# Optimization experiments

Measured on AMD Instinct MI355X. Metric: run time of the kernel, lower is better.

## Reference

```python
import jax, jax.numpy as jnp
import numpy as np

S = 8            # num_residual_streams (power of 2)
K = 3            # number of 2x2 Kronecker factors = log2(S)
T = 2 * K        # total_res_coeffs (2 permutations per 2x2 factor)
D = 2048         # feature dim per stream
B = 2            # batch
N = 1024         # sequence length


def setup_inputs() -> dict:
    key = jax.random.key(0)
    ks = jax.random.split(key, 6)
    residuals = jax.random.normal(ks[0], (B * S, N, D), dtype=jnp.float32)
    gamma = jnp.zeros((S * D,), dtype=jnp.float32)  # RMSNorm gamma (init zeros as in source)
    static_alpha = jax.random.normal(ks[1], (S + T,), dtype=jnp.float32)
    W_alpha = jax.random.normal(ks[2], (S * D, S + T), dtype=jnp.float32) * 0.02
    pre_branch_scale = jnp.full((1,), 0.01, dtype=jnp.float32)
    residual_scale = jnp.full((1,), 0.01, dtype=jnp.float32)
    static_beta = jax.random.normal(ks[3], (S,), dtype=jnp.float32)
    W_beta = jax.random.normal(ks[4], (S * D, S), dtype=jnp.float32) * 0.02
    h_post_scale = jnp.asarray(0.01, dtype=jnp.float32)
    return {"residuals": residuals, "gamma": gamma, "static_alpha": static_alpha,
            "W_alpha": W_alpha, "pre_branch_scale": pre_branch_scale,
            "residual_scale": residual_scale, "static_beta": static_beta,
            "W_beta": W_beta, "h_post_scale": h_post_scale}


def _kron_2x2(p):
    # p: (..., K) prob of identity for each 2x2 factor; U_k = [[p,1-p],[1-p,p]]
    q = 1.0 - p
    mats = jnp.stack([jnp.stack([p, q], axis=-1),
                      jnp.stack([q, p], axis=-1)], axis=-2)  # (..., K, 2, 2)
    out = mats[..., 0, :, :]
    for k in range(1, K):  # loop over fixed small K (structural), not data dims
        m = mats[..., k, :, :]
        a1, a2 = out.shape[-2], out.shape[-1]
        out = (out[..., :, None, :, None] * m[..., None, :, None, :]).reshape(
            *out.shape[:-2], a1 * 2, a2 * 2)
    return out  # (..., S, S) doubly stochastic Kronecker Hres


def reference(residuals, gamma, static_alpha, W_alpha, pre_branch_scale,
              residual_scale, static_beta, W_beta, h_post_scale):
    # residuals: (B*S, N, D) with stream-major layout '(b s) n d'
    r = residuals.reshape(B, S, N, D).transpose(0, 2, 1, 3)       # (B, N, S, D)
    flat = r.reshape(B, N, S * D)
    # RMSNorm: F.normalize(x, dim=-1) * sqrt(dim) * (gamma + 1)
    inv = jax.lax.rsqrt(jnp.maximum(jnp.sum(flat * flat, axis=-1, keepdims=True), 1e-24))
    normed = flat * inv * np.float32(np.sqrt(S * D)) * (gamma + 1.0)
    # dynamic-alpha projection: first S cols -> H_pre, last T cols -> Hres coeffs
    coeffs = normed @ W_alpha                                     # (B, N, S + T)
    dyn_pre, dyn_res = coeffs[..., :S], coeffs[..., S:]
    static_pre, static_res = static_alpha[:S], static_alpha[S:]
    # H_pre: softmax over streams -> convex-combination branch input
    w_pre = jax.nn.softmax(pre_branch_scale * dyn_pre + static_pre, axis=-1)
    branch_input = jnp.einsum('bns,bnsd->bnd', w_pre, r)
    # H_res: Kronecker product of 2x2 doubly-stochastic factor matrices
    cr = (residual_scale * dyn_res + static_res).reshape(B, N, K, 2)
    p = jax.nn.softmax(cr, axis=-1)[..., 0]                       # (B, N, K)
    hres = _kron_2x2(p)                                           # (B, N, S, S)
    mixed = jnp.einsum('bnst,bnsd->bntd', hres, r)                # stream mixing
    # branch = identity; depth connection with sigmoid-gated beta (H_post)
    beta = jax.nn.sigmoid(h_post_scale * (normed @ W_beta) + static_beta)  # (B, N, S)
    out = mixed + beta[..., None] * branch_input[..., None, :]    # (B, N, S, D)
    return out.transpose(0, 2, 1, 3).reshape(B * S, N, D)
```

## Files before the change

### kernel.cpp

```cpp
#include <hip/hip_runtime.h>
#include <stdint.h>

#define S_  8
#define D_  2048
#define B_  2
#define N_  1024
#define SD_ 16384
#define JP_ 11

__device__ __forceinline__ unsigned pack_bf16_rne(float a, float b) {
    unsigned ua = __float_as_uint(a);
    unsigned ub = __float_as_uint(b);
    ua += 0x7FFFu + ((ua >> 16) & 1u);
    ub += 0x7FFFu + ((ub >> 16) & 1u);
    return (ua >> 16) | (ub & 0xFFFF0000u);
}

extern "C" __global__ void krom_prep(const float* __restrict__ gamma,
                                     const float* __restrict__ Wa,
                                     const float* __restrict__ Wb,
                                     unsigned* __restrict__ Wp)
{
    const int u = blockIdx.x * 256 + threadIdx.x;
    if (u >= JP_ * SD_) return;
    const int sj = u >> 11;
    const int d  = u & 2047;
    const int s  = sj / JP_;
    const int jp = sj - s * JP_;
    const int i  = (s << 11) + d;
    const float g = gamma[i] + 1.0f;
    float w0, w1;
    if (jp < 7) {
        w0 = Wa[i * 14 + 2 * jp];
        w1 = Wa[i * 14 + 2 * jp + 1];
    } else {
        const int j = jp - 7;
        w0 = Wb[i * 8 + 2 * j];
        w1 = Wb[i * 8 + 2 * j + 1];
    }
    Wp[u] = pack_bf16_rne(g * w0, g * w1);
}

extern "C" __global__ void __launch_bounds__(512, 2)
krom_fused(const float* __restrict__ res,
           const unsigned* __restrict__ Wp,
           const float* __restrict__ sa,
           const float* __restrict__ pre_s,
           const float* __restrict__ res_s,
           const float* __restrict__ sb,
           const float* __restrict__ hps,
           float* __restrict__ out)
{
    const int tid = threadIdx.x;
    const int blk = blockIdx.x;
    const int b   = blk >> 9;
    const int n0  = (blk & 511) * 2;
    const int d0  = tid * 4;

    float acc0[23], acc1[23];
#pragma unroll
    for (int j = 0; j < 23; ++j) { acc0[j] = 0.0f; acc1[j] = 0.0f; }

    for (int s = 0; s < S_; ++s) {
        const float* pr = res + (((size_t)(b * S_ + s) * N_ + n0) * D_ + d0);
        const float4 va = *reinterpret_cast<const float4*>(pr);
        const float4 vb = *reinterpret_cast<const float4*>(pr + D_);
        const float ra[4] = {va.x, va.y, va.z, va.w};
        const float rb[4] = {vb.x, vb.y, vb.z, vb.w};
#pragma unroll
        for (int k = 0; k < 4; ++k) {
            acc0[22] = fmaf(ra[k], ra[k], acc0[22]);
            acc1[22] = fmaf(rb[k], rb[k], acc1[22]);
        }
        const unsigned* pw = Wp + ((s * JP_) << 11) + d0;
#pragma unroll
        for (int jp = 0; jp < JP_; ++jp) {
            const uint4 u = *reinterpret_cast<const uint4*>(pw + (jp << 11));
            const unsigned uu[4] = {u.x, u.y, u.z, u.w};
#pragma unroll
            for (int k = 0; k < 4; ++k) {
                const float w0 = __uint_as_float(uu[k] << 16);
                const float w1 = __uint_as_float(uu[k] & 0xFFFF0000u);
                acc0[2 * jp]     = fmaf(ra[k], w0, acc0[2 * jp]);
                acc0[2 * jp + 1] = fmaf(ra[k], w1, acc0[2 * jp + 1]);
                acc1[2 * jp]     = fmaf(rb[k], w0, acc1[2 * jp]);
                acc1[2 * jp + 1] = fmaf(rb[k], w1, acc1[2 * jp + 1]);
            }
        }
    }

    __shared__ float red[8][2][23];
    __shared__ float fin[2][23];
    const int wave = tid >> 6, lane = tid & 63;
#pragma unroll
    for (int j = 0; j < 23; ++j) {
        float v0 = acc0[j], v1 = acc1[j];
#pragma unroll
        for (int m = 1; m < 64; m <<= 1) {
            v0 += __shfl_xor(v0, m, 64);
            v1 += __shfl_xor(v1, m, 64);
        }
        if (lane == 0) { red[wave][0][j] = v0; red[wave][1][j] = v1; }
    }
    __syncthreads();
    if (tid < 46) {
        const int n = tid / 23, j = tid - n * 23;
        float v = 0.0f;
#pragma unroll
        for (int w = 0; w < 8; ++w) v += red[w][n][j];
        fin[n][j] = v;
    }
    __syncthreads();

    __shared__ float wpre[2][S_], bet[2][S_], pk3[2][3];
    if (tid < 2) {
        const int n = tid;
        const float inv   = rsqrtf(fmaxf(fin[n][22], 1e-24f));
        const float scale = inv * 128.0f;
        float c[22];
#pragma unroll
        for (int j = 0; j < 22; ++j) c[j] = fin[n][j] * scale;
        const float ps = pre_s[0], rs = res_s[0], hs = hps[0];
        float lg[8], mx = -1e30f;
#pragma unroll
        for (int s = 0; s < 8; ++s) { lg[s] = ps * c[s] + sa[s]; mx = fmaxf(mx, lg[s]); }
        float sum = 0.0f;
#pragma unroll
        for (int s = 0; s < 8; ++s) { lg[s] = expf(lg[s] - mx); sum += lg[s]; }
        const float rsum = 1.0f / sum;
#pragma unroll
        for (int s = 0; s < 8; ++s) wpre[n][s] = lg[s] * rsum;
#pragma unroll
        for (int k = 0; k < 3; ++k) {
            float a0 = rs * c[8 + 2 * k] + sa[8 + 2 * k];
            float a1 = rs * c[9 + 2 * k] + sa[9 + 2 * k];
            pk3[n][k] = 1.0f / (1.0f + expf(a1 - a0));
        }
#pragma unroll
        for (int t = 0; t < 8; ++t)
            bet[n][t] = 1.0f / (1.0f + expf(-(hs * c[14 + t] + sb[t])));
    }
    __syncthreads();

    __shared__ float Ms[2][S_][S_];
    if (tid < 128) {
        const int n = tid >> 6, e = tid & 63, s = e >> 3, t = e & 7;
        float h = 1.0f;
#pragma unroll
        for (int k = 0; k < 3; ++k) {
            int sbit = (s >> (2 - k)) & 1, tbit = (t >> (2 - k)) & 1;
            float pk = pk3[n][k];
            h *= (sbit == tbit) ? pk : (1.0f - pk);
        }
        Ms[n][s][t] = h + bet[n][t] * wpre[n][s];
    }
    __syncthreads();

#pragma unroll
    for (int n = 0; n < 2; ++n) {
        float o[8][4];
#pragma unroll
        for (int t = 0; t < 8; ++t)
#pragma unroll
            for (int k = 0; k < 4; ++k) o[t][k] = 0.0f;

        for (int s = 0; s < S_; ++s) {
            const float4 rv = *reinterpret_cast<const float4*>(
                res + (((size_t)(b * S_ + s) * N_ + (n0 + n)) * D_ + d0));
            const float4 m0 = *reinterpret_cast<const float4*>(&Ms[n][s][0]);
            const float4 m1 = *reinterpret_cast<const float4*>(&Ms[n][s][4]);
            o[0][0] = fmaf(m0.x, rv.x, o[0][0]); o[0][1] = fmaf(m0.x, rv.y, o[0][1]);
            o[0][2] = fmaf(m0.x, rv.z, o[0][2]); o[0][3] = fmaf(m0.x, rv.w, o[0][3]);
            o[1][0] = fmaf(m0.y, rv.x, o[1][0]); o[1][1] = fmaf(m0.y, rv.y, o[1][1]);
            o[1][2] = fmaf(m0.y, rv.z, o[1][2]); o[1][3] = fmaf(m0.y, rv.w, o[1][3]);
            o[2][0] = fmaf(m0.z, rv.x, o[2][0]); o[2][1] = fmaf(m0.z, rv.y, o[2][1]);
            o[2][2] = fmaf(m0.z, rv.z, o[2][2]); o[2][3] = fmaf(m0.z, rv.w, o[2][3]);
            o[3][0] = fmaf(m0.w, rv.x, o[3][0]); o[3][1] = fmaf(m0.w, rv.y, o[3][1]);
            o[3][2] = fmaf(m0.w, rv.z, o[3][2]); o[3][3] = fmaf(m0.w, rv.w, o[3][3]);
            o[4][0] = fmaf(m1.x, rv.x, o[4][0]); o[4][1] = fmaf(m1.x, rv.y, o[4][1]);
            o[4][2] = fmaf(m1.x, rv.z, o[4][2]); o[4][3] = fmaf(m1.x, rv.w, o[4][3]);
            o[5][0] = fmaf(m1.y, rv.x, o[5][0]); o[5][1] = fmaf(m1.y, rv.y, o[5][1]);
            o[5][2] = fmaf(m1.y, rv.z, o[5][2]); o[5][3] = fmaf(m1.y, rv.w, o[5][3]);
            o[6][0] = fmaf(m1.z, rv.x, o[6][0]); o[6][1] = fmaf(m1.z, rv.y, o[6][1]);
            o[6][2] = fmaf(m1.z, rv.z, o[6][2]); o[6][3] = fmaf(m1.z, rv.w, o[6][3]);
            o[7][0] = fmaf(m1.w, rv.x, o[7][0]); o[7][1] = fmaf(m1.w, rv.y, o[7][1]);
            o[7][2] = fmaf(m1.w, rv.z, o[7][2]); o[7][3] = fmaf(m1.w, rv.w, o[7][3]);
        }
#pragma unroll
        for (int t = 0; t < 8; ++t) {
            float* po = out + (((size_t)(b * S_ + t) * N_ + (n0 + n)) * D_ + d0);
            *reinterpret_cast<float4*>(po) = make_float4(o[t][0], o[t][1], o[t][2], o[t][3]);
        }
    }
}

extern "C" void kernel_launch(void* const* d_in, const int* in_sizes, int n_in,
                              void* d_out, int out_size, void* d_ws, size_t ws_size,
                              hipStream_t stream)
{
    (void)in_sizes; (void)n_in; (void)out_size; (void)ws_size;
    const float* residuals = (const float*)d_in[0];
    const float* gamma     = (const float*)d_in[1];
    const float* sa        = (const float*)d_in[2];
    const float* Wa        = (const float*)d_in[3];
    const float* pre_s     = (const float*)d_in[4];
    const float* res_s     = (const float*)d_in[5];
    const float* sb        = (const float*)d_in[6];
    const float* Wb        = (const float*)d_in[7];
    const float* hps       = (const float*)d_in[8];

    unsigned* Wp = (unsigned*)d_ws;

    hipLaunchKernelGGL(krom_prep, dim3((JP_ * SD_ + 255) / 256), dim3(256), 0, stream,
                       gamma, Wa, Wb, Wp);
    hipLaunchKernelGGL(krom_fused, dim3(B_ * N_ / 2), dim3(512), 0, stream,
                       residuals, Wp, sa, pre_s, res_s, sb, hps, (float*)d_out);
}
```

Before: 305.5 us.

## Process four tokens per block and use nontemporal output stores

Each block now handles four sequence positions instead of two, so every bf16 weight load feeds twice as many FMAs. This halves weight traffic per token and halves the grid to 512 blocks. Output writes switch to nontemporal stores so streaming output does not pollute the cache before residuals are re-read. The cost is more accumulator registers (92 versus 46), which may hurt occupancy under launch_bounds(512,2) and risks spilling, and fewer blocks to fill the GPU.

Result: no change. 304.4 us (-0.4%).

```diff
diff --git a/kernel.cpp b/kernel.cpp
--- a/kernel.cpp
+++ b/kernel.cpp
@@ -7,6 +7,9 @@
 #define N_  1024
 #define SD_ 16384
 #define JP_ 11
+#define NP_ 4
+
+typedef float f32x4 __attribute__((ext_vector_type(4)));
 
 __device__ __forceinline__ unsigned pack_bf16_rne(float a, float b) {
     unsigned ua = __float_as_uint(a);
@@ -53,24 +56,26 @@
 {
     const int tid = threadIdx.x;
     const int blk = blockIdx.x;
-    const int b   = blk >> 9;
-    const int n0  = (blk & 511) * 2;
+    const int b   = blk >> 8;
+    const int n0  = (blk & 255) * NP_;
     const int d0  = tid * 4;
 
-    float acc0[23], acc1[23];
-#pragma unroll
-    for (int j = 0; j < 23; ++j) { acc0[j] = 0.0f; acc1[j] = 0.0f; }
+    float acc[NP_][23];
+#pragma unroll
+    for (int n = 0; n < NP_; ++n)
+#pragma unroll
+        for (int j = 0; j < 23; ++j) acc[n][j] = 0.0f;
 
     for (int s = 0; s < S_; ++s) {
         const float* pr = res + (((size_t)(b * S_ + s) * N_ + n0) * D_ + d0);
-        const float4 va = *reinterpret_cast<const float4*>(pr);
-        const float4 vb = *reinterpret_cast<const float4*>(pr + D_);
-        const float ra[4] = {va.x, va.y, va.z, va.w};
-        const float rb[4] = {vb.x, vb.y, vb.z, vb.w};
-#pragma unroll
-        for (int k = 0; k < 4; ++k) {
-            acc0[22] = fmaf(ra[k], ra[k], acc0[22]);
-            acc1[22] = fmaf(rb[k], rb[k], acc1[22]);
+        float rr[NP_][4];
+#pragma unroll
+        for (int n = 0; n < NP_; ++n) {
+            const float4 v = *reinterpret_cast<const float4*>(pr + (size_t)n * D_);
+            rr[n][0] = v.x; rr[n][1] = v.y; rr[n][2] = v.z; rr[n][3] = v.w;
+#pragma unroll
+            for (int k = 0; k < 4; ++k)
+                acc[n][22] = fmaf(rr[n][k], rr[n][k], acc[n][22]);
         }
         const unsigned* pw = Wp + ((s * JP_) << 11) + d0;
 #pragma unroll
@@ -81,29 +86,29 @@
             for (int k = 0; k < 4; ++k) {
                 const float w0 = __uint_as_float(uu[k] << 16);
                 const float w1 = __uint_as_float(uu[k] & 0xFFFF0000u);
-                acc0[2 * jp]     = fmaf(ra[k], w0, acc0[2 * jp]);
-                acc0[2 * jp + 1] = fmaf(ra[k], w1, acc0[2 * jp + 1]);
-                acc1[2 * jp]     = fmaf(rb[k], w0, acc1[2 * jp]);
-                acc1[2 * jp + 1] = fmaf(rb[k], w1, acc1[2 * jp + 1]);
+#pragma unroll
+                for (int n = 0; n < NP_; ++n) {
+                    acc[n][2 * jp]     = fmaf(rr[n][k], w0, acc[n][2 * jp]);
+                    acc[n][2 * jp + 1] = fmaf(rr[n][k], w1, acc[n][2 * jp + 1]);
+                }
             }
         }
     }
 
-    __shared__ float red[8][2][23];
-    __shared__ float fin[2][23];
+    __shared__ float red[8][NP_][23];
+    __shared__ float fin[NP_][23];
     const int wave = tid >> 6, lane = tid & 63;
 #pragma unroll
-    for (int j = 0; j < 23; ++j) {
-        float v0 = acc0[j], v1 = acc1[j];
-#pragma unroll
-        for (int m = 1; m < 64; m <<= 1) {
-            v0 += __shfl_xor(v0, m, 64);
-            v1 += __shfl_xor(v1, m, 64);
-        }
-        if (lane == 0) { red[wave][0][j] = v0; red[wave][1][j] = v1; }
-    }
-    __syncthreads();
-    if (tid < 46) {
+    for (int n = 0; n < NP_; ++n)
+#pragma unroll
+        for (int j = 0; j < 23; ++j) {
+            float v = acc[n][j];
+#pragma unroll
+            for (int m = 1; m < 64; m <<= 1) v += __shfl_xor(v, m, 64);
+            if (lane == 0) red[wave][n][j] = v;
+        }
+    __syncthreads();
+    if (tid < NP_ * 23) {
         const int n = tid / 23, j = tid - n * 23;
         float v = 0.0f;
 #pragma unroll
@@ -112,8 +117,8 @@
     }
     __syncthreads();
 
-    __shared__ float wpre[2][S_], bet[2][S_], pk3[2][3];
-    if (tid < 2) {
+    __shared__ float wpre[NP_][S_], bet[NP_][S_], pk3[NP_][3];
+    if (tid < NP_) {
         const int n = tid;
         const float inv   = rsqrtf(fmaxf(fin[n][22], 1e-24f));
         const float scale = inv * 128.0f;
@@ -142,8 +147,8 @@
     }
     __syncthreads();
 
-    __shared__ float Ms[2][S_][S_];
-    if (tid < 128) {
+    __shared__ float Ms[NP_][S_][S_];
+    if (tid < NP_ * 64) {
         const int n = tid >> 6, e = tid & 63, s = e >> 3, t = e & 7;
         float h = 1.0f;
 #pragma unroll
@@ -157,7 +162,7 @@
     __syncthreads();
 
 #pragma unroll
-    for (int n = 0; n < 2; ++n) {
+    for (int n = 0; n < NP_; ++n) {
         float o[8][4];
 #pragma unroll
         for (int t = 0; t < 8; ++t)
@@ -189,7 +194,8 @@
 #pragma unroll
         for (int t = 0; t < 8; ++t) {
             float* po = out + (((size_t)(b * S_ + t) * N_ + (n0 + n)) * D_ + d0);
-            *reinterpret_cast<float4*>(po) = make_float4(o[t][0], o[t][1], o[t][2], o[t][3]);
+            f32x4 ov = {o[t][0], o[t][1], o[t][2], o[t][3]};
+            __builtin_nontemporal_store(ov, reinterpret_cast<f32x4*>(po));
         }
     }
 }
@@ -213,6 +219,6 @@
 
     hipLaunchKernelGGL(krom_prep, dim3((JP_ * SD_ + 255) / 256), dim3(256), 0, stream,
                        gamma, Wa, Wb, Wp);
-    hipLaunchKernelGGL(krom_fused, dim3(B_ * N_ / 2), dim3(512), 0, stream,
+    hipLaunchKernelGGL(krom_fused, dim3(B_ * N_ / NP_), dim3(512), 0, stream,
                        residuals, Wp, sa, pre_s, res_s, sb, hps, (float*)d_out);
 }
```
